# Performance work log

Hardware: AMD Instinct MI355X
Metric: run time of the kernel (lower is better)

The kernel has to match this reference:

```python
import jax, jax.numpy as jnp
import numpy as np

B, K, V, T, S, H = 128, 10, 50257, 20, 4, 2048  # batch, beam, vocab, seq_len, n_state, hidden


def setup_inputs() -> dict:
    key = jax.random.key(0)
    k1, k2, k3, k4, k5 = jax.random.split(key, 5)
    return {
        "logprobs": jax.random.normal(k1, (B, K, V), dtype=jnp.float32),
        "logprobs_sum": jax.random.normal(k2, (B, K), dtype=jnp.float32),
        "beam_seq_logprobs": jax.random.normal(k3, (B, T, K), dtype=jnp.float32),
        "state": jax.random.normal(k4, (B, S, K, H), dtype=jnp.float32),
        "beam_seq": jax.random.randint(k5, (B, T, K), 0, V, dtype=jnp.int64),
        "t": 5,
    }


def _beam_step(lp, lp_sum, seq, seq_lp, st, t):
    # lp: [K, V], lp_sum: [K], seq: [T, K] int, seq_lp: [T, K], st: [S, K, H]
    vocab = lp.shape[-1]
    # logprobsf[:, -1] -= 1000 (suppress EOS-like last token)
    lp = lp.at[:, vocab - 1].add(-1000.0)
    # group_size == 1 -> add_diversity is a no-op; unaug_logprobsf == lp.
    # torch.sort(logprobsf, 1, True) then take cols = beam_size per row == per-row top-k
    ys, ix = jax.lax.top_k(lp, K)  # [K(q), K(c)]
    # candidates appended with c outer, q inner -> flat index = c*K + q
    cand = lp_sum[:, None] + ys              # [q, c]
    flat = cand.T.reshape(-1)                # ordered as c*K + q
    order = jnp.argsort(-flat)[:K]           # stable descending sort, keep top beam
    c_sel = order // K
    q_sel = order % K
    tok = ix[q_sel, c_sel]                   # v['c']
    r = ys[q_sel, c_sel]                     # v['r'] (unaug == aug here)
    p = flat[order]                          # v['p']
    time_idx = jnp.arange(seq.shape[0])[:, None]
    # only rows < t are reordered from the parent beam; row t gets new entries
    new_seq = jnp.where(time_idx < t, seq[:, q_sel], seq).at[t].set(tok)
    new_seq_lp = jnp.where(time_idx < t, seq_lp[:, q_sel], seq_lp).at[t].set(r)
    new_state = st[:, q_sel, :]              # state gather/reorder on beam axis
    return new_seq, new_seq_lp, p, new_state


def reference(logprobs, logprobs_sum, beam_seq_logprobs, state, beam_seq, t):
    step = jax.vmap(_beam_step, in_axes=(0, 0, 0, 0, 0, None))
    return step(logprobs, logprobs_sum, beam_seq, beam_seq_logprobs, state, t)
```

## Files before the change

### kernel.cpp

```cpp
#include <hip/hip_runtime.h>
#include <math.h>
#include <stdint.h>

#define NB 128
#define NK 10
#define NV 50257
#define NT 20
#define NS 4
#define NH 2048

#define QCAP 576
#define QTRIG 48

__device__ __forceinline__ unsigned key_of(float f) {
    unsigned u = __float_as_uint(f);
    unsigned m = (unsigned)((int)u >> 31) | 0x80000000u;
    return u ^ m;
}
__device__ __forceinline__ float val_of(unsigned k) {
    unsigned m = (k & 0x80000000u) ? 0x80000000u : 0xFFFFFFFFu;
    return __uint_as_float(k ^ m);
}
__device__ __forceinline__ float rdlanef(float v, int l) {
    return __uint_as_float((unsigned)__builtin_amdgcn_readlane((int)__float_as_uint(v), l));
}

__global__ __launch_bounds__(256) void topk_rows(const float* __restrict__ lp,
                                                 float* __restrict__ ys,
                                                 int*   __restrict__ ix) {
    const int row  = blockIdx.x;
    const int tid  = threadIdx.x;
    const int lane = tid & 63;
    const int wave = tid >> 6;
    const float* rowp = lp + (size_t)row * NV;

    __shared__ unsigned long long Q[4][QCAP];
    __shared__ int qcnt[4];

    if (lane == 0) qcnt[wave] = 0;
    __threadfence_block();

    float thr = -INFINITY;

    auto lane_append = [&](float v, int idx) {
        if (v >= thr) {
            int p = atomicAdd(&qcnt[wave], 1);
            Q[wave][p] = ((unsigned long long)key_of(v) << 32) | (unsigned)(~(unsigned)idx);
        }
    };

    auto compact = [&]() {
        __threadfence_block();
        int cnt = qcnt[wave];
        if (cnt > 10) {
            if (cnt <= 64) {
                unsigned long long mine = (lane < cnt) ? Q[wave][lane] : 0ull;
                int rk = 0;
                for (int j = 0; j < cnt; ++j)
                    rk += (Q[wave][j] > mine) ? 1 : 0;
                __threadfence_block();
                if (lane < cnt && rk < 10) Q[wave][rk] = mine;
            } else {
                unsigned long long mine[9];
                int rk[9];
#pragma unroll
                for (int s = 0; s < 9; ++s) {
                    int e = lane + (s << 6);
                    mine[s] = (e < cnt) ? Q[wave][e] : 0ull;
                    rk[s] = 0;
                }
                for (int j = 0; j < cnt; ++j) {
                    unsigned long long qv = Q[wave][j];
#pragma unroll
                    for (int s = 0; s < 9; ++s) rk[s] += (qv > mine[s]) ? 1 : 0;
                }
                __threadfence_block();
#pragma unroll
                for (int s = 0; s < 9; ++s) {
                    int e = lane + (s << 6);
                    if (e < cnt && rk[s] < 10) Q[wave][rk[s]] = mine[s];
                }
            }
            if (lane == 0) qcnt[wave] = 10;
            __threadfence_block();
            thr = val_of((unsigned)(Q[wave][9] >> 32));
        }
    };

    auto process8 = [&](float4 a, float4 b, int basea) {
        float m8 = fmaxf(fmaxf(fmaxf(a.x, a.y), fmaxf(a.z, a.w)),
                         fmaxf(fmaxf(b.x, b.y), fmaxf(b.z, b.w)));
        if (__ballot(m8 >= thr)) {
            lane_append(a.x, basea + 0);
            lane_append(a.y, basea + 1);
            lane_append(a.z, basea + 2);
            lane_append(a.w, basea + 3);
            lane_append(b.x, basea + 1024);
            lane_append(b.y, basea + 1025);
            lane_append(b.z, basea + 1026);
            lane_append(b.w, basea + 1027);
            __threadfence_block();
            if (qcnt[wave] >= QTRIG) compact();
        }
    };

    const int head = (int)(((16u - (unsigned)((uintptr_t)rowp & 15u)) & 15u) >> 2);
    const int n4 = (NV - 1 - head) >> 2;
    const int NFULL = n4 >> 9;
    const float4* rowp4 = (const float4*)(rowp + head);

    float4 a0 = rowp4[tid];
    float4 b0 = rowp4[tid + 256];
    float4 pa = rowp4[512 + tid];
    float4 pb = rowp4[768 + tid];

    float m8 = fmaxf(fmaxf(fmaxf(a0.x, a0.y), fmaxf(a0.z, a0.w)),
                     fmaxf(fmaxf(b0.x, b0.y), fmaxf(b0.z, b0.w)));
    int rank = 0;
    for (int j = 0; j < 64; ++j) {
        float o = rdlanef(m8, j);
        rank += ((o > m8) || (o == m8 && j < lane)) ? 1 : 0;
    }
    {
        unsigned long long b9 = __ballot(rank == 9);
        int l9 = (int)__builtin_ctzll(b9);
        thr = rdlanef(m8, l9);
    }
    {
        int basea = head + 4 * tid;
        lane_append(a0.x, basea + 0);
        lane_append(a0.y, basea + 1);
        lane_append(a0.z, basea + 2);
        lane_append(a0.w, basea + 3);
        lane_append(b0.x, basea + 1024);
        lane_append(b0.y, basea + 1025);
        lane_append(b0.z, basea + 1026);
        lane_append(b0.w, basea + 1027);
        __threadfence_block();
        if (qcnt[wave] >= QTRIG) compact();
    }

    for (int it = 1; it < NFULL; ++it) {
        float4 ca = pa, cb = pb;
        if (it + 1 < NFULL) {
            pa = rowp4[((it + 1) << 9) + tid];
            pb = rowp4[((it + 1) << 9) + 256 + tid];
        }
        process8(ca, cb, head + 4 * ((it << 9) + tid));
    }
    {
        int ja = (NFULL << 9) + tid;
        int jb = ja + 256;
        float4 a = (ja < n4) ? rowp4[ja]
                             : make_float4(-INFINITY, -INFINITY, -INFINITY, -INFINITY);
        float4 b = (jb < n4) ? rowp4[jb]
                             : make_float4(-INFINITY, -INFINITY, -INFINITY, -INFINITY);
        process8(a, b, head + 4 * ja);
    }
    if (wave == 0) {
        if (lane < head) lane_append(rowp[lane], lane);
        int idx = head + 4 * n4 + lane;
        if (idx < NV) {
            float v = rowp[idx];
            if (idx == NV - 1) v -= 1000.0f;
            lane_append(v, idx);
        }
    }

    compact();
    __syncthreads();

    if (tid < 40) {
        int w = tid / 10, r = tid - w * 10;
        unsigned long long my = Q[w][r];
        int rnk = 0;
#pragma unroll
        for (int w2 = 0; w2 < 4; ++w2)
            for (int r2 = 0; r2 < 10; ++r2)
                rnk += (Q[w2][r2] > my) ? 1 : 0;
        if (rnk < 10) {
            ys[row * 10 + rnk] = val_of((unsigned)(my >> 32));
            ix[row * 10 + rnk] = (int)(~(unsigned)(my & 0xFFFFFFFFull));
        }
    }
}

__global__ __launch_bounds__(256) void select_gather(
    const float* __restrict__ lp_sum,
    const float* __restrict__ seq_lp,
    const int*   __restrict__ seq,
    const int*   __restrict__ tptr,
    const float* __restrict__ ys,
    const int*   __restrict__ ix,
    const float* __restrict__ st,
    float* __restrict__ out_seq,
    float* __restrict__ out_seq_lp,
    float* __restrict__ out_p,
    float* __restrict__ out_st)
{
    const int row = blockIdx.x;
    const int b   = row / (NS * NK);
    const int rem = row - b * (NS * NK);
    const int s   = rem / NK;
    const int k   = rem - s * NK;
    const int tid = threadIdx.x;

    __shared__ float sf[100];
    __shared__ int   so[10];
    __shared__ int   sq[10];
    __shared__ int   stok[10];
    __shared__ float sr[10];

    if (tid < 100) {
        int c = tid / 10, q = tid % 10;
        sf[tid] = lp_sum[b * 10 + q] + ys[(b * 10 + q) * 10 + c];
    }
    __syncthreads();
    if (tid < 100) {
        float v = sf[tid];
        int rank = 0;
        for (int j = 0; j < 100; ++j) {
            float u = sf[j];
            rank += (u > v || (u == v && j < tid)) ? 1 : 0;
        }
        if (rank < 10) so[rank] = tid;
    }
    __syncthreads();

    const int q = so[k] % 10;
    const float4* src = (const float4*)(st + ((size_t)(b * NS + s) * NK + q) * NH);
    float4*       dst = (float4*)(out_st + (size_t)row * NH);
    dst[tid]       = src[tid];
    dst[tid + 256] = src[tid + 256];

    if (s == 0 && k == 0) {
        const int t = tptr[0];
        if (tid < 10) {
            int f = so[tid];
            int c = f / 10, qq = f % 10;
            sq[tid]   = qq;
            stok[tid] = ix[(b * 10 + qq) * 10 + c];
            sr[tid]   = ys[(b * 10 + qq) * 10 + c];
            out_p[b * 10 + tid] = sf[f];
        }
        __syncthreads();
        if (tid < NT * NK) {
            int time = tid / 10, kk = tid % 10;
            int qs = sq[kk];
            int src_k = (time < t) ? qs : kk;
            int   sval = seq[(b * NT + time) * 10 + src_k];
            float lv = seq_lp[(b * NT + time) * 10 + src_k];
            if (time == t) { sval = stok[kk]; lv = sr[kk]; }
            out_seq[(b * NT + time) * 10 + kk]    = (float)sval;
            out_seq_lp[(b * NT + time) * 10 + kk] = lv;
        }
    }
}

extern "C" void kernel_launch(void* const* d_in, const int* in_sizes, int n_in,
                              void* d_out, int out_size, void* d_ws, size_t ws_size,
                              hipStream_t stream) {
    const float* lp      = (const float*)d_in[0];
    const float* lp_sum  = (const float*)d_in[1];
    const float* seq_lp  = (const float*)d_in[2];
    const float* st      = (const float*)d_in[3];
    const int*   seq     = (const int*)d_in[4];
    const int*   tptr    = (const int*)d_in[5];

    float* out        = (float*)d_out;
    float* out_seq    = out;
    float* out_seq_lp = out + NB * NT * NK;
    float* out_p      = out + 2 * NB * NT * NK;
    float* out_st     = out + 2 * NB * NT * NK + NB * NK;

    float* ws_ys   = (float*)d_ws;
    int*   ws_ix   = (int*)((char*)d_ws + 51200);

    topk_rows<<<NB * NK, 256, 0, stream>>>(lp, ws_ys, ws_ix);
    select_gather<<<NB * NS * NK, 256, 0, stream>>>(
        lp_sum, seq_lp, seq, tptr, ws_ys, ws_ix, st,
        out_seq, out_seq_lp, out_p, out_st);
}
```

Before: 68.93 us.

## Deepen topk prefetch to two stages and coarsen state gather per block

```diff
diff --git a/kernel.cpp b/kernel.cpp
--- a/kernel.cpp
+++ b/kernel.cpp
@@ -109,10 +109,12 @@
     const int NFULL = n4 >> 9;
     const float4* rowp4 = (const float4*)(rowp + head);
 
-    float4 a0 = rowp4[tid];
-    float4 b0 = rowp4[tid + 256];
-    float4 pa = rowp4[512 + tid];
-    float4 pb = rowp4[768 + tid];
+    float4 a0  = rowp4[tid];
+    float4 b0  = rowp4[tid + 256];
+    float4 p0a = rowp4[512 + tid];
+    float4 p0b = rowp4[768 + tid];
+    float4 p1a = rowp4[1024 + tid];
+    float4 p1b = rowp4[1280 + tid];
 
     float m8 = fmaxf(fmaxf(fmaxf(a0.x, a0.y), fmaxf(a0.z, a0.w)),
                      fmaxf(fmaxf(b0.x, b0.y), fmaxf(b0.z, b0.w)));
@@ -141,10 +143,11 @@
     }
 
     for (int it = 1; it < NFULL; ++it) {
-        float4 ca = pa, cb = pb;
-        if (it + 1 < NFULL) {
-            pa = rowp4[((it + 1) << 9) + tid];
-            pb = rowp4[((it + 1) << 9) + 256 + tid];
+        float4 ca = p0a, cb = p0b;
+        p0a = p1a; p0b = p1b;
+        if (it + 2 < NFULL) {
+            p1a = rowp4[((it + 2) << 9) + tid];
+            p1b = rowp4[((it + 2) << 9) + 256 + tid];
         }
         process8(ca, cb, head + 4 * ((it << 9) + tid));
     }
@@ -198,11 +201,9 @@
     float* __restrict__ out_p,
     float* __restrict__ out_st)
 {
-    const int row = blockIdx.x;
-    const int b   = row / (NS * NK);
-    const int rem = row - b * (NS * NK);
-    const int s   = rem / NK;
-    const int k   = rem - s * NK;
+    const int bs  = blockIdx.x;
+    const int b   = bs / NS;
+    const int s   = bs - b * NS;
     const int tid = threadIdx.x;
 
     __shared__ float sf[100];
@@ -227,13 +228,27 @@
     }
     __syncthreads();
 
-    const int q = so[k] % 10;
-    const float4* src = (const float4*)(st + ((size_t)(b * NS + s) * NK + q) * NH);
-    float4*       dst = (float4*)(out_st + (size_t)row * NH);
-    dst[tid]       = src[tid];
-    dst[tid + 256] = src[tid + 256];
-
-    if (s == 0 && k == 0) {
+    const float* src_base = st + (size_t)bs * NK * NH;
+    float*       dst_base = out_st + (size_t)bs * NK * NH;
+#pragma unroll
+    for (int kk = 0; kk < 10; kk += 2) {
+        const int q0 = so[kk] % 10;
+        const int q1 = so[kk + 1] % 10;
+        const float4* s0 = (const float4*)(src_base + (size_t)q0 * NH);
+        const float4* s1 = (const float4*)(src_base + (size_t)q1 * NH);
+        float4 x0 = s0[tid];
+        float4 x1 = s0[tid + 256];
+        float4 y0 = s1[tid];
+        float4 y1 = s1[tid + 256];
+        float4* d0 = (float4*)(dst_base + (size_t)kk * NH);
+        float4* d1 = (float4*)(dst_base + (size_t)(kk + 1) * NH);
+        d0[tid]       = x0;
+        d0[tid + 256] = x1;
+        d1[tid]       = y0;
+        d1[tid + 256] = y1;
+    }
+
+    if (s == 0) {
         const int t = tptr[0];
         if (tid < 10) {
             int f = so[tid];
@@ -277,7 +292,7 @@
     int*   ws_ix   = (int*)((char*)d_ws + 51200);
 
     topk_rows<<<NB * NK, 256, 0, stream>>>(lp, ws_ys, ws_ix);
-    select_gather<<<NB * NS * NK, 256, 0, stream>>>(
+    select_gather<<<NB * NS, 256, 0, stream>>>(
         lp_sum, seq_lp, seq, tptr, ws_ys, ws_ix, st,
         out_seq, out_seq_lp, out_p, out_st);
 }
```

After: 64.81 us (median of 2 runs). 1.06x faster.
